# Optimization experiments

Hardware: AMD Instinct MI355X
Metric: run time of the kernel (lower is better)

## Reference

```python
import jax, jax.numpy as jnp
import numpy as np

B_, H_, N_, L_ = 4, 512, 64, 2048  # batch, d_model, d_state/2 (conj pairs), seq len


def setup_inputs() -> dict:
    key = jax.random.key(0)
    ks = jax.random.split(key, 8)
    x = jax.random.normal(ks[0], (B_, H_, L_), jnp.float32)
    ln_w = jnp.ones((H_,), jnp.float32)
    ln_b = jnp.zeros((H_,), jnp.float32)
    # S4D-style init: dt log-uniform in [1e-3, 1e-1], A = -1/2 + i*pi*n (S4D-Lin)
    log_dt = jax.random.uniform(ks[1], (H_,), jnp.float32) * (np.log(0.1) - np.log(0.001)) + np.log(0.001)
    log_A_real = jnp.broadcast_to(jnp.log(jnp.float32(0.5)), (H_, N_))
    A_imag = jnp.broadcast_to(np.pi * jnp.arange(N_, dtype=np.float32), (H_, N_))
    B_re = jnp.ones((H_, N_), jnp.float32)
    B_im = jnp.zeros((H_, N_), jnp.float32)
    # 2 kernel channels for bidirectional
    C_re = jax.random.normal(ks[2], (2, H_, N_), jnp.float32) * (0.5 ** 0.5)
    C_im = jax.random.normal(ks[3], (2, H_, N_), jnp.float32) * (0.5 ** 0.5)
    D = jax.random.normal(ks[4], (H_,), jnp.float32)
    W_out = jax.random.normal(ks[5], (H_, H_), jnp.float32) / np.sqrt(H_)
    b_out = jnp.zeros((H_,), jnp.float32)
    return dict(x=x, ln_w=ln_w, ln_b=ln_b, log_dt=log_dt, log_A_real=log_A_real,
                A_imag=A_imag, B_re=B_re, B_im=B_im, C_re=C_re, C_im=C_im,
                D=D, W_out=W_out, b_out=b_out)


def _s4_layer(x, ln_w, ln_b, log_dt, log_A_real, A_imag, B_re, B_im, C_re, C_im, D, W_out, b_out):
    Bb, H, L = x.shape
    # ---- pre-norm LayerNorm over channel dim (module transposes to (B,L,H)) ----
    zt = x.transpose(0, 2, 1)                          # (B, L, H)
    mu = zt.mean(-1, keepdims=True)
    var = jnp.mean((zt - mu) ** 2, -1, keepdims=True)
    zt = (zt - mu) * jax.lax.rsqrt(var + 1e-5) * ln_w + ln_b
    z = zt.transpose(0, 2, 1)                          # (B, H, L)
    # ---- S4 diagonal SSM kernel, ZOH discretization, 2 channels (bidirectional) ----
    dt = jnp.exp(log_dt)[:, None]                      # (H, 1)
    A = -jnp.exp(log_A_real) + 1j * A_imag             # (H, N)
    dtA = A * dt                                       # (H, N)
    dB = (B_re + 1j * B_im) * (jnp.exp(dtA) - 1.0) / A # (H, N) discretized B
    CB = (C_re + 1j * C_im) * dB                       # (2, H, N)
    V = jnp.exp(dtA[:, :, None] * jnp.arange(L))       # (H, N, L) Vandermonde exp(l*dt*A)
    k = 2.0 * jnp.real(jnp.einsum('chn,hnl->chl', CB, V))  # (2, H, L)
    # ---- bidirectional: causal + flipped anticausal kernel, length 2L ----
    zpad = jnp.zeros_like(k[0])
    kb = jnp.concatenate([k[0], zpad], -1) + jnp.concatenate([zpad, k[1][:, ::-1]], -1)  # (H, 2L)
    # ---- FFT convolution ----
    k_f = jnp.fft.rfft(kb, n=2 * L)                    # (H, L+1)
    u_f = jnp.fft.rfft(z, n=2 * L)                     # (B, H, L+1)
    y = jnp.fft.irfft(u_f * k_f, n=2 * L)[..., :L]     # (B, H, L)
    y = y + z * D[:, None]                             # skip connection D*u
    y = jax.nn.gelu(y)                                 # default S4 activation
    y = jnp.einsum('oh,bhl->bol', W_out, y) + b_out[:, None]  # output linear (Conv1d k=1)
    return y + x                                       # residual of S4Layer


def reference(x, ln_w, ln_b, log_dt, log_A_real, A_imag, B_re, B_im, C_re, C_im, D, W_out, b_out):
    return _s4_layer(x, ln_w, ln_b, log_dt, log_A_real, A_imag, B_re, B_im, C_re, C_im, D, W_out, b_out)
```

## Files before the change

### kernel.cpp

```cpp
#include <hip/hip_runtime.h>
#include <math.h>

#define Bq 4
#define Hq 512
#define Nq 64
#define Lq 2048
#define PARAM (Hq*Nq)
#define T 64
#define NC (Lq/T)
#define NCOL 256

__global__ __launch_bounds__(256)
void setup_kernel(const float* __restrict__ log_dt,
                  const float* __restrict__ log_A_real,
                  const float* __restrict__ A_imag,
                  const float* __restrict__ B_re, const float* __restrict__ B_im,
                  const float* __restrict__ C_re, const float* __restrict__ C_im,
                  float* __restrict__ a0, float* __restrict__ b0,
                  float* __restrict__ a1, float* __restrict__ b1,
                  float* __restrict__ pw, float* __restrict__ pwT,
                  const float* __restrict__ x, const float* __restrict__ lnw,
                  const float* __restrict__ lnb, float* __restrict__ z) {
    __shared__ float rs_[16][17], r2_[16][17], mu_s[16], sg_s[16];
    int bx = blockIdx.x;
    if (bx < 128) {
        int idx = bx * 256 + threadIdx.x;
        int h = idx >> 6, n = idx & 63;
        float dt = expf(log_dt[h]);
        float Ar = -expf(log_A_real[idx]);
        float Ai = A_imag[idx];
        float er = expf(Ar * dt);
        float wr = er * cosf(Ai * dt);
        float wi = er * sinf(Ai * dt);
        float mr = wr - 1.0f, mi = wi;
        float den = Ar * Ar + Ai * Ai;
        float qr = (mr * Ar + mi * Ai) / den;
        float qi = (mi * Ar - mr * Ai) / den;
        float Br = B_re[idx], Bi = B_im[idx];
        float dBr = Br * qr - Bi * qi;
        float dBi = Br * qi + Bi * qr;
        float cr = C_re[idx], ci = C_im[idx];
        a0[idx] =  2.0f * (cr * dBr - ci * dBi);
        b0[idx] = -2.0f * (cr * dBi + ci * dBr);
        cr = C_re[PARAM + idx]; ci = C_im[PARAM + idx];
        a1[idx] =  2.0f * (cr * dBr - ci * dBi);
        b1[idx] = -2.0f * (cr * dBi + ci * dBr);
        float c = 1.f, s = 0.f;
        float* base  = pw  + (size_t)h * 65 * 128 + 2 * n;
        float* baseT = pwT + (size_t)(h * 64 + n) * 132;
        for (int d = 0; d <= 64; ++d) {
            *(float2*)(base + (size_t)d * 128) = float2{c, s};
            *(float2*)(baseT + 2 * d)          = float2{c, s};
            float nc = c * wr - s * wi;
            float ns = c * wi + s * wr;
            c = nc; s = ns;
        }
        return;
    }
    int blk = bx - 128;
    int b  = blk / (Lq / 16);
    int l0 = (blk % (Lq / 16)) * 16;
    int tx = threadIdx.x & 15;
    int ty = threadIdx.x >> 4;
    const float* xb = x + (size_t)b * Hq * Lq;
    float s = 0.f, s2 = 0.f;
    for (int h = ty; h < Hq; h += 16) {
        float v = xb[h * Lq + l0 + tx];
        s += v; s2 += v * v;
    }
    rs_[ty][tx] = s; r2_[ty][tx] = s2;
    __syncthreads();
    if (ty == 0) {
        float a = 0.f, c = 0.f;
        #pragma unroll
        for (int i = 0; i < 16; ++i) { a += rs_[i][tx]; c += r2_[i][tx]; }
        float mu = a * (1.0f / Hq);
        float var = c * (1.0f / Hq) - mu * mu;
        mu_s[tx] = mu;
        sg_s[tx] = rsqrtf(var + 1e-5f);
    }
    __syncthreads();
    float mu = mu_s[tx], rs = sg_s[tx];
    float* zb = z + (size_t)b * Hq * Lq;
    for (int h = ty; h < Hq; h += 16) {
        float v = xb[h * Lq + l0 + tx];
        zb[h * Lq + l0 + tx] = (v - mu) * rs * lnw[h] + lnb[h];
    }
}

__global__ __launch_bounds__(256, 3)
void deltascan_kernel(const float* __restrict__ z, const float* __restrict__ pw,
                      const float* __restrict__ a0, const float* __restrict__ b0,
                      const float* __restrict__ a1, const float* __restrict__ b1,
                      float* __restrict__ kt, float* __restrict__ buf) {
    __shared__ float Bs[64][68];
    __shared__ float Ds[64][130];
    int h = blockIdx.x;
    int t = threadIdx.x;
    if (blockIdx.y == 4) {
        if (t < 128) {
            int dir = t >> 6, d = t & 63;
            const float* aa = dir ? a1 : a0;
            const float* bb = dir ? b1 : b0;
            const float* row = pw + (size_t)(h * 65 + d) * 128;
            float acc = 0.f;
            for (int n = 0; n < 64; ++n) {
                float2 v = *(const float2*)(row + 2 * n);
                acc = fmaf(aa[h * 64 + n], v.x, acc);
                acc = fmaf(bb[h * 64 + n], v.y, acc);
            }
            kt[((size_t)h * 2 + dir) * 64 + d] = acc;
        }
        return;
    }
    int ct = blockIdx.y;
    int dir = ct >> 1;
    int cc = t & 31, rb = (t >> 5) & 1, jg = t >> 6;
    int b = (ct & 1) * 2 + rb;
    const float* zb = z + ((size_t)b * Hq + h) * Lq;
    if (dir == 0) {
        #pragma unroll
        for (int f = 0; f < 4; ++f) {
            float4 v = *(const float4*)(zb + cc * 64 + 16 * jg + 4 * f);
            Bs[16*jg+4*f+0][rb*32+cc] = v.x;
            Bs[16*jg+4*f+1][rb*32+cc] = v.y;
            Bs[16*jg+4*f+2][rb*32+cc] = v.z;
            Bs[16*jg+4*f+3][rb*32+cc] = v.w;
        }
    } else {
        #pragma unroll
        for (int f = 0; f < 4; ++f) {
            float4 v = *(const float4*)(zb + 2044 - cc * 64 - 16 * jg - 4 * f);
            Bs[16*jg+4*f+3][rb*32+cc] = v.x;
            Bs[16*jg+4*f+2][rb*32+cc] = v.y;
            Bs[16*jg+4*f+1][rb*32+cc] = v.z;
            Bs[16*jg+4*f+0][rb*32+cc] = v.w;
        }
    }
    __syncthreads();
    int tx = t & 15, ty = t >> 4;
    float aR[4][4] = {}, aI[4][4] = {};
    const float* pwh = pw + (size_t)h * 65 * 128;
    #pragma unroll 4
    for (int kk = 0; kk < 64; ++kk) {
        int d = 63 - kk;
        const float4* pr = (const float4*)(pwh + (size_t)d * 128 + 8 * tx);
        float4 p0 = pr[0], p1 = pr[1];
        float4 bv = *(const float4*)&Bs[kk][4 * ty];
        float pc[4] = {p0.x, p0.z, p1.x, p1.z};
        float ps[4] = {p0.y, p0.w, p1.y, p1.w};
        #pragma unroll
        for (int rr = 0; rr < 4; ++rr) {
            #pragma unroll
            for (int q = 0; q < 4; ++q) {
                aR[rr][q] = fmaf(pc[rr], (&bv.x)[q], aR[rr][q]);
                aI[rr][q] = fmaf(ps[rr], (&bv.x)[q], aI[rr][q]);
            }
        }
    }
    #pragma unroll
    for (int q = 0; q < 4; ++q) {
        float* dst = &Ds[4 * ty + q][8 * tx];
        float4 v1, v2;
        v1.x = aR[0][q]; v1.y = aI[0][q]; v1.z = aR[1][q]; v1.w = aI[1][q];
        v2.x = aR[2][q]; v2.y = aI[2][q]; v2.z = aR[3][q]; v2.w = aI[3][q];
        *(float4*)dst = v1; *(float4*)(dst + 4) = v2;
    }
    __syncthreads();
    if (t < 128) {
        int bl = t >> 6, n = t & 63;
        float2 w64 = *(const float2*)(pw + (size_t)(h * 65 + 64) * 128 + 2 * n);
        float tc = w64.x, ts = w64.y;
        float sr = 0.f, si = 0.f;
        #pragma unroll 4
        for (int c = 0; c < NC; ++c) {
            int col = bl * 32 + c;
            float dr = Ds[col][2 * n], di = Ds[col][2 * n + 1];
            Ds[col][2 * n] = sr; Ds[col][2 * n + 1] = si;
            float nr = fmaf(tc, sr, fmaf(-ts, si, dr));
            float ni = fmaf(ts, sr, fmaf(tc, si, di));
            sr = nr; si = ni;
        }
    }
    __syncthreads();
    int colo = t >> 2, qg = t & 3;
    const float* srcd = &Ds[colo][qg * 32];
    float* dstg = buf + ((size_t)h * NCOL + ct * 64 + colo) * 128 + qg * 32;
    #pragma unroll
    for (int f = 0; f < 8; ++f)
        *(float4*)(dstg + 4 * f) = *(const float4*)(srcd + 4 * f);
}

__global__ __launch_bounds__(256, 4)
void yact_kernel(const float* __restrict__ z, const float* __restrict__ pwT,
                 const float* __restrict__ a0, const float* __restrict__ b0,
                 const float* __restrict__ a1, const float* __restrict__ b1,
                 const float* __restrict__ kt, const float* __restrict__ buf,
                 const float* __restrict__ Dv, float* __restrict__ u) {
    __shared__ float As[64][68];
    __shared__ float Bs[64][68];
    __shared__ float ks0[64], ks1[64], as0_[64], bs0_[64], as1_[64], bs1_[64];
    int h = blockIdx.x, bp = blockIdx.y;
    int t = threadIdx.x;
    if (t < 64) {
        ks0[t]  = kt[((size_t)h * 2 + 0) * 64 + t];
        ks1[t]  = kt[((size_t)h * 2 + 1) * 64 + t];
        as0_[t] = a0[h * 64 + t]; bs0_[t] = b0[h * 64 + t];
        as1_[t] = a1[h * 64 + t]; bs1_[t] = b1[h * 64 + t];
    }
    int tx = t & 15, ty = t >> 4;
    int si = t & 63, kg = t >> 6;
    int bS = 2 * bp + (si >> 5), ch = si & 31;
    const float* zb   = z + ((size_t)bS * Hq + h) * Lq + ch * 64;
    const float* bufh = buf + (size_t)h * NCOL * 128;
    const float* buf0 = bufh + (size_t)(bS * 32 + ch) * 128;
    const float* buf1 = bufh + (size_t)(128 + bS * 32 + (31 - ch)) * 128;
    const float* pwh  = pwT + (size_t)h * 64 * 132;
    float4 rB[4];
    float2 pv[8];
    #pragma unroll
    for (int f = 0; f < 4; ++f)
        rB[f] = *(const float4*)(zb + 16 * kg + 4 * f);
    float acc[4][4] = {};
    __syncthreads();
    for (int p = 0; p < 5; ++p) {
        if (p == 0) {
            #pragma unroll
            for (int q = 0; q < 16; ++q) {
                int kk = 16 * kg + q;
                int d = si - kk;
                As[kk][si] = (d >= 0) ? ks0[d] : ks1[-d - 1];
            }
        } else {
            const float* as_ = (p < 3) ? as0_ : as1_;
            const float* bs_ = (p < 3) ? bs0_ : bs1_;
            #pragma unroll
            for (int q = 0; q < 16; ++q) {
                int j = q >> 1;
                int n = 32 * ((p < 3) ? (p - 1) : (p - 3)) + 8 * kg + j;
                float vx = pv[j].x, vy = pv[j].y;
                As[16 * kg + q][si] = ((q & 1) == 0)
                    ? fmaf(as_[n], vx, bs_[n] * vy)
                    : fmaf(bs_[n], vx, -as_[n] * vy);
            }
        }
        #pragma unroll
        for (int f = 0; f < 4; ++f) {
            Bs[16*kg + 4*f + 0][si] = rB[f].x;
            Bs[16*kg + 4*f + 1][si] = rB[f].y;
            Bs[16*kg + 4*f + 2][si] = rB[f].z;
            Bs[16*kg + 4*f + 3][si] = rB[f].w;
        }
        __syncthreads();
        if (p < 4) {
            int pn = p + 1;
            int pp = (pn < 3) ? (pn - 1) : (pn - 3);
            const float* src = (pn < 3) ? buf0 : buf1;
            #pragma unroll
            for (int f = 0; f < 4; ++f)
                rB[f] = *(const float4*)(src + 64 * pp + 16 * kg + 4 * f);
            int dsel = (pn < 3) ? (si + 1) : (63 - si);
            #pragma unroll
            for (int j = 0; j < 8; ++j) {
                int n = 32 * pp + 8 * kg + j;
                pv[j] = *(const float2*)(pwh + (size_t)n * 132 + 2 * dsel);
            }
        }
        #pragma unroll 8
        for (int kk = 0; kk < 64; ++kk) {
            float4 av = *(const float4*)&As[kk][4 * tx];
            float4 bv = *(const float4*)&Bs[kk][4 * ty];
            #pragma unroll
            for (int ii = 0; ii < 4; ++ii) {
                float a = (&av.x)[ii];
                acc[ii][0] = fmaf(a, bv.x, acc[ii][0]);
                acc[ii][1] = fmaf(a, bv.y, acc[ii][1]);
                acc[ii][2] = fmaf(a, bv.z, acc[ii][2]);
                acc[ii][3] = fmaf(a, bv.w, acc[ii][3]);
            }
        }
        __syncthreads();
    }
    float dv = Dv[h];
    #pragma unroll
    for (int q = 0; q < 4; ++q) {
        int cc2 = 4 * ty + q;
        int b2 = 2 * bp + (cc2 >> 5), ch2 = cc2 & 31;
        size_t base = ((size_t)b2 * Hq + h) * Lq + ch2 * 64 + 4 * tx;
        float4 zr = *(const float4*)(z + base);
        float vv[4];
        vv[0] = acc[0][q] + dv * zr.x;
        vv[1] = acc[1][q] + dv * zr.y;
        vv[2] = acc[2][q] + dv * zr.z;
        vv[3] = acc[3][q] + dv * zr.w;
        #pragma unroll
        for (int i = 0; i < 4; ++i) {
            float v = vv[i];
            float tt = tanhf(0.7978845608028654f * (v + 0.044715f * v * v * v));
            vv[i] = 0.5f * v * (1.0f + tt);
        }
        float4 r; r.x = vv[0]; r.y = vv[1]; r.z = vv[2]; r.w = vv[3];
        *(float4*)(u + base) = r;
    }
}

__global__ __launch_bounds__(512, 4)
void gemm_kernel(const float* __restrict__ u, const float* __restrict__ W,
                 const float* __restrict__ bias, const float* __restrict__ x,
                 float* __restrict__ out) {
    int l0 = blockIdx.x * 64;
    int o0 = blockIdx.y * 128;
    int b  = blockIdx.z;
    int tid = threadIdx.x;
    __shared__ float Ws[2][32][132];
    __shared__ float Us[2][32][68];
    const float* ub = u + (size_t)b * Hq * Lq;
    float acc[4][4] = {};
    int wo = tid >> 4, wl = tid & 15;
    int sj = tid & 31, so = tid >> 5;
    int sl = tid & 63, sk = tid >> 6;
    float wreg[8], ureg[4];
    #pragma unroll
    for (int r = 0; r < 8; ++r) wreg[r] = W[(size_t)(o0 + so + 16*r) * Hq + sj];
    #pragma unroll
    for (int r = 0; r < 4; ++r) ureg[r] = ub[(size_t)(4*sk + r) * Lq + l0 + sl];
    #pragma unroll
    for (int r = 0; r < 8; ++r) Ws[0][sj][so + 16*r] = wreg[r];
    #pragma unroll
    for (int r = 0; r < 4; ++r) Us[0][4*sk + r][sl] = ureg[r];
    __syncthreads();
    for (int t = 0; t < Hq / 32; ++t) {
        int cur = t & 1;
        if (t < 15) {
            int k0 = (t + 1) * 32;
            #pragma unroll
            for (int r = 0; r < 8; ++r)
                wreg[r] = W[(size_t)(o0 + so + 16*r) * Hq + k0 + sj];
            #pragma unroll
            for (int r = 0; r < 4; ++r)
                ureg[r] = ub[(size_t)(k0 + 4*sk + r) * Lq + l0 + sl];
        }
        #pragma unroll 8
        for (int j = 0; j < 32; ++j) {
            float4 av = *(const float4*)&Ws[cur][j][4 * wo];
            float4 bv = *(const float4*)&Us[cur][j][4 * wl];
            #pragma unroll
            for (int io = 0; io < 4; ++io) {
                float a = (&av.x)[io];
                acc[io][0] = fmaf(a, bv.x, acc[io][0]);
                acc[io][1] = fmaf(a, bv.y, acc[io][1]);
                acc[io][2] = fmaf(a, bv.z, acc[io][2]);
                acc[io][3] = fmaf(a, bv.w, acc[io][3]);
            }
        }
        if (t < 15) {
            int nxt = cur ^ 1;
            #pragma unroll
            for (int r = 0; r < 8; ++r) Ws[nxt][sj][so + 16*r] = wreg[r];
            #pragma unroll
            for (int r = 0; r < 4; ++r) Us[nxt][4*sk + r][sl] = ureg[r];
        }
        __syncthreads();
    }
    #pragma unroll
    for (int io = 0; io < 4; ++io) {
        int o = o0 + 4 * wo + io;
        float bo = bias[o];
        size_t base = ((size_t)b * Hq + o) * Lq + l0 + 4 * wl;
        const float4 xr = *(const float4*)(x + base);
        float4 r;
        r.x = acc[io][0] + bo + xr.x;
        r.y = acc[io][1] + bo + xr.y;
        r.z = acc[io][2] + bo + xr.z;
        r.w = acc[io][3] + bo + xr.w;
        *(float4*)(out + base) = r;
    }
}

extern "C" void kernel_launch(void* const* d_in, const int* in_sizes, int n_in,
                              void* d_out, int out_size, void* d_ws, size_t ws_size,
                              hipStream_t stream) {
    (void)in_sizes; (void)n_in; (void)out_size; (void)ws_size;
    const float* x          = (const float*)d_in[0];
    const float* ln_w       = (const float*)d_in[1];
    const float* ln_b       = (const float*)d_in[2];
    const float* log_dt     = (const float*)d_in[3];
    const float* log_A_real = (const float*)d_in[4];
    const float* A_imag     = (const float*)d_in[5];
    const float* B_re       = (const float*)d_in[6];
    const float* B_im       = (const float*)d_in[7];
    const float* C_re       = (const float*)d_in[8];
    const float* C_im       = (const float*)d_in[9];
    const float* Dv         = (const float*)d_in[10];
    const float* W          = (const float*)d_in[11];
    const float* b_out      = (const float*)d_in[12];
    float* out = (float*)d_out;
    float* ws  = (float*)d_ws;

    const size_t BHL = (size_t)Bq * Hq * Lq;
    float* a0  = ws;
    float* b0  = ws + (size_t)PARAM;
    float* a1  = ws + 2 * (size_t)PARAM;
    float* b1  = ws + 3 * (size_t)PARAM;
    float* kt  = ws + 4 * (size_t)PARAM;
    float* pw  = ws + 6 * (size_t)PARAM;
    float* pwT = ws + 136 * (size_t)PARAM;
    float* z   = ws + 268 * (size_t)PARAM;
    float* u   = z  + BHL;
    float* buf = u + BHL;

    setup_kernel<<<128 + Bq * (Lq / 16), 256, 0, stream>>>(
        log_dt, log_A_real, A_imag, B_re, B_im, C_re, C_im,
        a0, b0, a1, b1, pw, pwT, x, ln_w, ln_b, z);
    deltascan_kernel<<<dim3(Hq, 5), 256, 0, stream>>>(z, pw, a0, b0, a1, b1,
                                                      kt, buf);
    yact_kernel<<<dim3(Hq, 2), 256, 0, stream>>>(z, pwT, a0, b0, a1, b1,
                                                 kt, buf, Dv, u);
    gemm_kernel<<<dim3(Lq / 64, Hq / 128, Bq), 512, 0, stream>>>(u, W, b_out, x, out);
}
```

Baseline: 299.4 us.

## Fuse chunk-state scan into SSM output kernel and drop intermediate buffer

Merges the deltascan and yact kernels into a single ssm_kernel. Each block now computes the per-chunk state contributions for both directions in registers, runs a two-level scan (within thread, then across thread groups in shared memory using the squared-squared twiddle), and feeds the resulting states straight into the chunked output GEMM. The kernel-tap vector is also computed inside the block. This removes one launch and the global round-trip through the buf and kt arrays, at the cost of more registers per thread, an extra GEMM pass per block, and fewer blocks (1024 instead of 2560 in the first stage).

```diff
diff --git a/kernel.cpp b/kernel.cpp
--- a/kernel.cpp
+++ b/kernel.cpp
@@ -6,9 +6,6 @@
 #define Nq 64
 #define Lq 2048
 #define PARAM (Hq*Nq)
-#define T 64
-#define NC (Lq/T)
-#define NCOL 256
 
 __global__ __launch_bounds__(256)
 void setup_kernel(const float* __restrict__ log_dt,
@@ -89,147 +86,160 @@
 }
 
 __global__ __launch_bounds__(256, 3)
-void deltascan_kernel(const float* __restrict__ z, const float* __restrict__ pw,
-                      const float* __restrict__ a0, const float* __restrict__ b0,
-                      const float* __restrict__ a1, const float* __restrict__ b1,
-                      float* __restrict__ kt, float* __restrict__ buf) {
-    __shared__ float Bs[64][68];
-    __shared__ float Ds[64][130];
-    int h = blockIdx.x;
-    int t = threadIdx.x;
-    if (blockIdx.y == 4) {
-        if (t < 128) {
-            int dir = t >> 6, d = t & 63;
-            const float* aa = dir ? a1 : a0;
-            const float* bb = dir ? b1 : b0;
-            const float* row = pw + (size_t)(h * 65 + d) * 128;
-            float acc = 0.f;
-            for (int n = 0; n < 64; ++n) {
-                float2 v = *(const float2*)(row + 2 * n);
-                acc = fmaf(aa[h * 64 + n], v.x, acc);
-                acc = fmaf(bb[h * 64 + n], v.y, acc);
-            }
-            kt[((size_t)h * 2 + dir) * 64 + d] = acc;
-        }
-        return;
-    }
-    int ct = blockIdx.y;
-    int dir = ct >> 1;
-    int cc = t & 31, rb = (t >> 5) & 1, jg = t >> 6;
-    int b = (ct & 1) * 2 + rb;
-    const float* zb = z + ((size_t)b * Hq + h) * Lq;
-    if (dir == 0) {
-        #pragma unroll
-        for (int f = 0; f < 4; ++f) {
-            float4 v = *(const float4*)(zb + cc * 64 + 16 * jg + 4 * f);
-            Bs[16*jg+4*f+0][rb*32+cc] = v.x;
-            Bs[16*jg+4*f+1][rb*32+cc] = v.y;
-            Bs[16*jg+4*f+2][rb*32+cc] = v.z;
-            Bs[16*jg+4*f+3][rb*32+cc] = v.w;
-        }
-    } else {
-        #pragma unroll
-        for (int f = 0; f < 4; ++f) {
-            float4 v = *(const float4*)(zb + 2044 - cc * 64 - 16 * jg - 4 * f);
-            Bs[16*jg+4*f+3][rb*32+cc] = v.x;
-            Bs[16*jg+4*f+2][rb*32+cc] = v.y;
-            Bs[16*jg+4*f+1][rb*32+cc] = v.z;
-            Bs[16*jg+4*f+0][rb*32+cc] = v.w;
-        }
-    }
-    __syncthreads();
-    int tx = t & 15, ty = t >> 4;
-    float aR[4][4] = {}, aI[4][4] = {};
-    const float* pwh = pw + (size_t)h * 65 * 128;
-    #pragma unroll 4
-    for (int kk = 0; kk < 64; ++kk) {
-        int d = 63 - kk;
-        const float4* pr = (const float4*)(pwh + (size_t)d * 128 + 8 * tx);
-        float4 p0 = pr[0], p1 = pr[1];
-        float4 bv = *(const float4*)&Bs[kk][4 * ty];
-        float pc[4] = {p0.x, p0.z, p1.x, p1.z};
-        float ps[4] = {p0.y, p0.w, p1.y, p1.w};
-        #pragma unroll
-        for (int rr = 0; rr < 4; ++rr) {
-            #pragma unroll
-            for (int q = 0; q < 4; ++q) {
-                aR[rr][q] = fmaf(pc[rr], (&bv.x)[q], aR[rr][q]);
-                aI[rr][q] = fmaf(ps[rr], (&bv.x)[q], aI[rr][q]);
-            }
-        }
-    }
-    #pragma unroll
-    for (int q = 0; q < 4; ++q) {
-        float* dst = &Ds[4 * ty + q][8 * tx];
-        float4 v1, v2;
-        v1.x = aR[0][q]; v1.y = aI[0][q]; v1.z = aR[1][q]; v1.w = aI[1][q];
-        v2.x = aR[2][q]; v2.y = aI[2][q]; v2.z = aR[3][q]; v2.w = aI[3][q];
-        *(float4*)dst = v1; *(float4*)(dst + 4) = v2;
-    }
-    __syncthreads();
-    if (t < 128) {
-        int bl = t >> 6, n = t & 63;
-        float2 w64 = *(const float2*)(pw + (size_t)(h * 65 + 64) * 128 + 2 * n);
-        float tc = w64.x, ts = w64.y;
-        float sr = 0.f, si = 0.f;
-        #pragma unroll 4
-        for (int c = 0; c < NC; ++c) {
-            int col = bl * 32 + c;
-            float dr = Ds[col][2 * n], di = Ds[col][2 * n + 1];
-            Ds[col][2 * n] = sr; Ds[col][2 * n + 1] = si;
-            float nr = fmaf(tc, sr, fmaf(-ts, si, dr));
-            float ni = fmaf(ts, sr, fmaf(tc, si, di));
-            sr = nr; si = ni;
-        }
-    }
-    __syncthreads();
-    int colo = t >> 2, qg = t & 3;
-    const float* srcd = &Ds[colo][qg * 32];
-    float* dstg = buf + ((size_t)h * NCOL + ct * 64 + colo) * 128 + qg * 32;
-    #pragma unroll
-    for (int f = 0; f < 8; ++f)
-        *(float4*)(dstg + 4 * f) = *(const float4*)(srcd + 4 * f);
-}
-
-__global__ __launch_bounds__(256, 4)
-void yact_kernel(const float* __restrict__ z, const float* __restrict__ pwT,
-                 const float* __restrict__ a0, const float* __restrict__ b0,
-                 const float* __restrict__ a1, const float* __restrict__ b1,
-                 const float* __restrict__ kt, const float* __restrict__ buf,
-                 const float* __restrict__ Dv, float* __restrict__ u) {
+void ssm_kernel(const float* __restrict__ z, const float* __restrict__ pw,
+                const float* __restrict__ pwT,
+                const float* __restrict__ a0, const float* __restrict__ b0,
+                const float* __restrict__ a1, const float* __restrict__ b1,
+                const float* __restrict__ Dv, float* __restrict__ u) {
+    __shared__ float Zs[64][68];
     __shared__ float As[64][68];
-    __shared__ float Bs[64][68];
     __shared__ float ks0[64], ks1[64], as0_[64], bs0_[64], as1_[64], bs1_[64];
     int h = blockIdx.x, bp = blockIdx.y;
     int t = threadIdx.x;
+    int tx = t & 15, ty = t >> 4;
+    const float* pwh  = pw  + (size_t)h * 65 * 128;
+    const float* pwTh = pwT + (size_t)h * 64 * 132;
+    {
+        int cc = t & 31, rb = (t >> 5) & 1, jg = t >> 6;
+        const float* zb = z + ((size_t)(2 * bp + rb) * Hq + h) * Lq;
+        #pragma unroll
+        for (int f = 0; f < 4; ++f) {
+            float4 v = *(const float4*)(zb + cc * 64 + 16 * jg + 4 * f);
+            Zs[16*jg+4*f+0][rb*32+cc] = v.x;
+            Zs[16*jg+4*f+1][rb*32+cc] = v.y;
+            Zs[16*jg+4*f+2][rb*32+cc] = v.z;
+            Zs[16*jg+4*f+3][rb*32+cc] = v.w;
+        }
+    }
     if (t < 64) {
-        ks0[t]  = kt[((size_t)h * 2 + 0) * 64 + t];
-        ks1[t]  = kt[((size_t)h * 2 + 1) * 64 + t];
-        as0_[t] = a0[h * 64 + t]; bs0_[t] = b0[h * 64 + t];
-        as1_[t] = a1[h * 64 + t]; bs1_[t] = b1[h * 64 + t];
-    }
-    int tx = t & 15, ty = t >> 4;
+        as0_[t] = a0[h*64+t]; bs0_[t] = b0[h*64+t];
+        as1_[t] = a1[h*64+t]; bs1_[t] = b1[h*64+t];
+    }
+    __syncthreads();
+    if (t < 128) {
+        int dir_ = t >> 6, d = t & 63;
+        float acc2 = 0.f;
+        if (dir_ == 0) {
+            for (int n = 0; n < 64; ++n) {
+                float2 v = *(const float2*)(pwTh + (size_t)n*132 + 2*d);
+                acc2 = fmaf(as0_[n], v.x, acc2);
+                acc2 = fmaf(bs0_[n], v.y, acc2);
+            }
+            ks0[d] = acc2;
+        } else {
+            for (int n = 0; n < 64; ++n) {
+                float2 v = *(const float2*)(pwTh + (size_t)n*132 + 2*d);
+                acc2 = fmaf(as1_[n], v.x, acc2);
+                acc2 = fmaf(bs1_[n], v.y, acc2);
+            }
+            ks1[d] = acc2;
+        }
+    }
+    float d0R[4][4] = {}, d0I[4][4] = {}, d1R[4][4] = {}, d1I[4][4] = {};
+    #pragma unroll 2
+    for (int j = 0; j < 64; ++j) {
+        const float4* prA = (const float4*)(pwh + (size_t)(63-j)*128 + 8*tx);
+        const float4* prB = (const float4*)(pwh + (size_t)j*128 + 8*tx);
+        float4 pA0 = prA[0], pA1 = prA[1];
+        float4 pB0 = prB[0], pB1 = prB[1];
+        float4 zv = *(const float4*)&Zs[j][4*ty];
+        float cA[4] = {pA0.x, pA0.z, pA1.x, pA1.z};
+        float sA[4] = {pA0.y, pA0.w, pA1.y, pA1.w};
+        float cB[4] = {pB0.x, pB0.z, pB1.x, pB1.z};
+        float sB[4] = {pB0.y, pB0.w, pB1.y, pB1.w};
+        #pragma unroll
+        for (int rr = 0; rr < 4; ++rr) {
+            #pragma unroll
+            for (int q = 0; q < 4; ++q) {
+                float zq = (&zv.x)[q];
+                d0R[rr][q] = fmaf(cA[rr], zq, d0R[rr][q]);
+                d0I[rr][q] = fmaf(sA[rr], zq, d0I[rr][q]);
+                d1R[rr][q] = fmaf(cB[rr], zq, d1R[rr][q]);
+                d1I[rr][q] = fmaf(sB[rr], zq, d1I[rr][q]);
+            }
+        }
+    }
+    const float4* pr64 = (const float4*)(pwh + (size_t)64*128 + 8*tx);
+    float4 w0v = pr64[0], w1v = pr64[1];
+    float wc[4] = {w0v.x, w0v.z, w1v.x, w1v.z};
+    float wn[4] = {w0v.y, w0v.w, w1v.y, w1v.w};
+    int bS = ty >> 3, g = ty & 7;
+    float* Vs = &As[0][0];
+    #pragma unroll
+    for (int rr = 0; rr < 4; ++rr) {
+        float vr = 0.f, vi = 0.f;
+        #pragma unroll
+        for (int q = 0; q < 4; ++q) {
+            float nr = fmaf(wc[rr], vr, fmaf(-wn[rr], vi, d0R[rr][q]));
+            float ni = fmaf(wn[rr], vr, fmaf(wc[rr], vi, d0I[rr][q]));
+            vr = nr; vi = ni;
+        }
+        *(float2*)(Vs + (size_t)((bS)*8+g)*130 + 2*(4*tx+rr)) = float2{vr, vi};
+        vr = 0.f; vi = 0.f;
+        #pragma unroll
+        for (int q = 3; q >= 0; --q) {
+            float nr = fmaf(wc[rr], vr, fmaf(-wn[rr], vi, d1R[rr][q]));
+            float ni = fmaf(wn[rr], vr, fmaf(wc[rr], vi, d1I[rr][q]));
+            vr = nr; vi = ni;
+        }
+        *(float2*)(Vs + (size_t)((2+bS)*8+g)*130 + 2*(4*tx+rr)) = float2{vr, vi};
+    }
+    __syncthreads();
+    {
+        int dir_ = t >> 7, bS_ = (t >> 6) & 1, n_ = t & 63;
+        float2 wv = *(const float2*)(pwh + (size_t)64*128 + 2*n_);
+        float w2r = fmaf(wv.x, wv.x, -(wv.y*wv.y));
+        float w2i = 2.f*wv.x*wv.y;
+        float Tr = fmaf(w2r, w2r, -(w2i*w2i));
+        float Ti = 2.f*w2r*w2i;
+        float* row = Vs + (size_t)(dir_*2+bS_)*8*130 + 2*n_;
+        float er = 0.f, ei = 0.f;
+        #pragma unroll
+        for (int s2 = 0; s2 < 8; ++s2) {
+            int g2 = dir_ ? (7 - s2) : s2;
+            float* p2 = row + g2*130;
+            float vr2 = p2[0], vi2 = p2[1];
+            p2[0] = er; p2[1] = ei;
+            float nr = fmaf(Tr, er, fmaf(-Ti, ei, vr2));
+            float ni = fmaf(Ti, er, fmaf(Tr, ei, vi2));
+            er = nr; ei = ni;
+        }
+    }
+    __syncthreads();
+    #pragma unroll
+    for (int rr = 0; rr < 4; ++rr) {
+        float2 E0 = *(const float2*)(Vs + (size_t)((bS)*8+g)*130 + 2*(4*tx+rr));
+        float trr = E0.x, tii = E0.y;
+        #pragma unroll
+        for (int q = 0; q < 4; ++q) {
+            float dr = d0R[rr][q], di = d0I[rr][q];
+            d0R[rr][q] = trr; d0I[rr][q] = tii;
+            float nr = fmaf(wc[rr], trr, fmaf(-wn[rr], tii, dr));
+            float ni = fmaf(wn[rr], trr, fmaf(wc[rr], tii, di));
+            trr = nr; tii = ni;
+        }
+        float2 E1 = *(const float2*)(Vs + (size_t)((2+bS)*8+g)*130 + 2*(4*tx+rr));
+        trr = E1.x; tii = E1.y;
+        #pragma unroll
+        for (int q = 3; q >= 0; --q) {
+            float dr = d1R[rr][q], di = d1I[rr][q];
+            d1R[rr][q] = trr; d1I[rr][q] = tii;
+            float nr = fmaf(wc[rr], trr, fmaf(-wn[rr], tii, dr));
+            float ni = fmaf(wn[rr], trr, fmaf(wc[rr], tii, di));
+            trr = nr; tii = ni;
+        }
+    }
+    __syncthreads();
     int si = t & 63, kg = t >> 6;
-    int bS = 2 * bp + (si >> 5), ch = si & 31;
-    const float* zb   = z + ((size_t)bS * Hq + h) * Lq + ch * 64;
-    const float* bufh = buf + (size_t)h * NCOL * 128;
-    const float* buf0 = bufh + (size_t)(bS * 32 + ch) * 128;
-    const float* buf1 = bufh + (size_t)(128 + bS * 32 + (31 - ch)) * 128;
-    const float* pwh  = pwT + (size_t)h * 64 * 132;
-    float4 rB[4];
     float2 pv[8];
-    #pragma unroll
-    for (int f = 0; f < 4; ++f)
-        rB[f] = *(const float4*)(zb + 16 * kg + 4 * f);
     float acc[4][4] = {};
-    __syncthreads();
     for (int p = 0; p < 5; ++p) {
         if (p == 0) {
             #pragma unroll
             for (int q = 0; q < 16; ++q) {
-                int kk = 16 * kg + q;
+                int kk = 16*kg + q;
                 int d = si - kk;
-                As[kk][si] = (d >= 0) ? ks0[d] : ks1[-d - 1];
+                As[kk][si] = (d >= 0) ? ks0[d] : ks1[-d-1];
             }
         } else {
             const float* as_ = (p < 3) ? as0_ : as1_;
@@ -237,39 +247,68 @@
             #pragma unroll
             for (int q = 0; q < 16; ++q) {
                 int j = q >> 1;
-                int n = 32 * ((p < 3) ? (p - 1) : (p - 3)) + 8 * kg + j;
+                int n = 32*((p < 3) ? (p-1) : (p-3)) + 8*kg + j;
                 float vx = pv[j].x, vy = pv[j].y;
-                As[16 * kg + q][si] = ((q & 1) == 0)
-                    ? fmaf(as_[n], vx, bs_[n] * vy)
-                    : fmaf(bs_[n], vx, -as_[n] * vy);
-            }
-        }
-        #pragma unroll
-        for (int f = 0; f < 4; ++f) {
-            Bs[16*kg + 4*f + 0][si] = rB[f].x;
-            Bs[16*kg + 4*f + 1][si] = rB[f].y;
-            Bs[16*kg + 4*f + 2][si] = rB[f].z;
-            Bs[16*kg + 4*f + 3][si] = rB[f].w;
+                As[16*kg+q][si] = ((q&1) == 0) ? fmaf(as_[n], vx, bs_[n]*vy)
+                                               : fmaf(bs_[n], vx, -as_[n]*vy);
+            }
+            if (p == 1 && tx < 8) {
+                #pragma unroll
+                for (int rr = 0; rr < 4; ++rr) {
+                    int ml = 8*tx + 2*rr;
+                    #pragma unroll
+                    for (int q = 0; q < 4; ++q) {
+                        Zs[ml][4*ty+q]   = d0R[rr][q];
+                        Zs[ml+1][4*ty+q] = d0I[rr][q];
+                    }
+                }
+            } else if (p == 2 && tx >= 8) {
+                #pragma unroll
+                for (int rr = 0; rr < 4; ++rr) {
+                    int ml = 8*(tx-8) + 2*rr;
+                    #pragma unroll
+                    for (int q = 0; q < 4; ++q) {
+                        Zs[ml][4*ty+q]   = d0R[rr][q];
+                        Zs[ml+1][4*ty+q] = d0I[rr][q];
+                    }
+                }
+            } else if (p == 3 && tx < 8) {
+                #pragma unroll
+                for (int rr = 0; rr < 4; ++rr) {
+                    int ml = 8*tx + 2*rr;
+                    #pragma unroll
+                    for (int q = 0; q < 4; ++q) {
+                        Zs[ml][4*ty+q]   = d1R[rr][q];
+                        Zs[ml+1][4*ty+q] = d1I[rr][q];
+                    }
+                }
+            } else if (p == 4 && tx >= 8) {
+                #pragma unroll
+                for (int rr = 0; rr < 4; ++rr) {
+                    int ml = 8*(tx-8) + 2*rr;
+                    #pragma unroll
+                    for (int q = 0; q < 4; ++q) {
+                        Zs[ml][4*ty+q]   = d1R[rr][q];
+                        Zs[ml+1][4*ty+q] = d1I[rr][q];
+                    }
+                }
+            }
         }
         __syncthreads();
         if (p < 4) {
             int pn = p + 1;
-            int pp = (pn < 3) ? (pn - 1) : (pn - 3);
-            const float* src = (pn < 3) ? buf0 : buf1;
-            #pragma unroll
-            for (int f = 0; f < 4; ++f)
-                rB[f] = *(const float4*)(src + 64 * pp + 16 * kg + 4 * f);
+            int pp = (pn < 3) ? (pn-1) : (pn-3);
             int dsel = (pn < 3) ? (si + 1) : (63 - si);
             #pragma unroll
-            for (int j = 0; j < 8; ++j) {
-                int n = 32 * pp + 8 * kg + j;
-                pv[j] = *(const float2*)(pwh + (size_t)n * 132 + 2 * dsel);
+            for (int j2 = 0; j2 < 8; ++j2) {
+                int n = 32*pp + 8*kg + j2;
+                pv[j2] = *(const float2*)(pwTh + (size_t)n*132 + 2*dsel);
             }
         }
         #pragma unroll 8
         for (int kk = 0; kk < 64; ++kk) {
-            float4 av = *(const float4*)&As[kk][4 * tx];
-            float4 bv = *(const float4*)&Bs[kk][4 * ty];
+            float4 av = *(const float4*)&As[kk][4*tx];
+            float4 bv = *(const float4*)&Zs[kk][4*ty];
             #pragma unroll
             for (int ii = 0; ii < 4; ++ii) {
                 float a = (&av.x)[ii];
@@ -284,8 +323,8 @@
     float dv = Dv[h];
     #pragma unroll
     for (int q = 0; q < 4; ++q) {
-        int cc2 = 4 * ty + q;
-        int b2 = 2 * bp + (cc2 >> 5), ch2 = cc2 & 31;
+        int cc2 = 4*ty + q;
+        int b2 = 2*bp + (cc2 >> 5), ch2 = cc2 & 31;
         size_t base = ((size_t)b2 * Hq + h) * Lq + ch2 * 64 + 4 * tx;
         float4 zr = *(const float4*)(z + base);
         float vv[4];
@@ -402,19 +441,15 @@
     float* b0  = ws + (size_t)PARAM;
     float* a1  = ws + 2 * (size_t)PARAM;
     float* b1  = ws + 3 * (size_t)PARAM;
-    float* kt  = ws + 4 * (size_t)PARAM;
-    float* pw  = ws + 6 * (size_t)PARAM;
-    float* pwT = ws + 136 * (size_t)PARAM;
-    float* z   = ws + 268 * (size_t)PARAM;
-    float* u   = z  + BHL;
-    float* buf = u + BHL;
+    float* pw  = ws + 4 * (size_t)PARAM;
+    float* pwT = ws + 134 * (size_t)PARAM;
+    float* z   = ws + 266 * (size_t)PARAM;
+    float* u   = z + BHL;
 
     setup_kernel<<<128 + Bq * (Lq / 16), 256, 0, stream>>>(
         log_dt, log_A_real, A_imag, B_re, B_im, C_re, C_im,
         a0, b0, a1, b1, pw, pwT, x, ln_w, ln_b, z);
-    deltascan_kernel<<<dim3(Hq, 5), 256, 0, stream>>>(z, pw, a0, b0, a1, b1,
-                                                      kt, buf);
-    yact_kernel<<<dim3(Hq, 2), 256, 0, stream>>>(z, pwT, a0, b0, a1, b1,
-                                                 kt, buf, Dv, u);
+    ssm_kernel<<<dim3(Hq, 2), 256, 0, stream>>>(z, pw, pwT, a0, b0, a1, b1,
+                                                Dv, u);
     gemm_kernel<<<dim3(Lq / 64, Hq / 128, Bq), 512, 0, stream>>>(u, W, b_out, x, out);
 }
```

Result: faster. 281.1 us (-6.1%).
